# Kernel optimization log

Measured on AMD Instinct MI355X. Metric: run time of the kernel, lower is better.

Reference implementation:

```python
import jax, jax.numpy as jnp
import numpy as np

V, OOV, E, HE, HD, B, S, T = 50000, 100, 128, 256, 256, 32, 256, 16
NEG = -1e20


def lstm(x, W, U, b, h0, c0):
    # x: [B, L, F]; standard (Keras-style i,f,g,o) LSTM via scan over time
    def step(carry, xt):
        h, c = carry
        z = xt @ W + h @ U + b
        i, f, g, o = jnp.split(z, 4, axis=-1)
        c = jax.nn.sigmoid(f) * c + jax.nn.sigmoid(i) * jnp.tanh(g)
        h = jax.nn.sigmoid(o) * jnp.tanh(c)
        return (h, c), h
    (h, c), hs = jax.lax.scan(step, (h0, c0), jnp.swapaxes(x, 0, 1))
    return jnp.swapaxes(hs, 0, 1), h, c


def setup_inputs() -> dict:
    key = jax.random.key(0)
    ks = jax.random.split(key, 16)
    g = lambda i, shape: jax.random.normal(ks[i], shape, dtype=jnp.float32) * 0.05
    return {
        'x': jax.random.randint(ks[0], (B, S), 0, V),
        'x_with_oov': jax.random.randint(ks[1], (B, S), 0, V + OOV),
        'x_len': jax.random.randint(ks[2], (B,), 1, S + 1),
        'dec_x': jax.random.randint(ks[3], (B, T), 0, V),
        'embedding': g(4, (V, E)),
        'Wenc': g(5, (E, 4 * HE)), 'Uenc': g(6, (HE, 4 * HE)), 'benc': jnp.zeros(4 * HE, jnp.float32),
        'We2d': g(7, (HE, HD)), 'be2d': jnp.zeros(HD, jnp.float32),
        'Wdec': g(8, (E, 4 * HD)), 'Udec': g(9, (HD, 4 * HD)), 'bdec': jnp.zeros(4 * HD, jnp.float32),
        'Wattn': g(10, (HD, HE)),
        'Wout': g(11, (HE + HD, HD)), 'bout': jnp.zeros(HD, jnp.float32),
        'Wgen': g(12, (HD, V)),
        'Wcopy': g(13, (HE, HD)), 'bcopy': jnp.zeros(HD, jnp.float32),
    }


def reference(x, x_with_oov, x_len, dec_x, embedding, Wenc, Uenc, benc,
              We2d, be2d, Wdec, Udec, bdec, Wattn, Wout, bout, Wgen, Wcopy, bcopy):
    # Encoder (unidirectional; Keras encoder ignores mask in this branch)
    enc_out, eh, ec = lstm(embedding[x], Wenc, Uenc, benc,
                           jnp.zeros((B, HE), embedding.dtype), jnp.zeros((B, HE), embedding.dtype))
    # NOTE: source applies encoder2decoder_state to BOTH h and c (faithful)
    h0 = eh @ We2d + be2d
    c0 = ec @ We2d + be2d
    # Decoder LSTM
    dec_out, sh, sc = lstm(embedding[dec_x], Wdec, Udec, bdec, h0, c0)  # [B,T,HD]
    mask = jnp.arange(S)[None, :] < x_len[:, None]                      # [B,S]
    # Attention (score_mode='general')
    scores = jnp.einsum('bth,he,bse->bts', dec_out, Wattn, enc_out)     # [B,T,S]
    scores = jnp.where(mask[:, None, :], scores, NEG)
    aw = jax.nn.softmax(scores, axis=2)
    ctx = jnp.einsum('bts,bse->bte', aw, enc_out)                       # [B,T,HE]
    attn_out = jnp.tanh(jnp.concatenate([ctx, dec_out], axis=-1) @ Wout + bout)  # [B,T,HD]
    # Generation scores, padded with tiny constant over OOV slots
    gen = jnp.exp(attn_out @ Wgen)                                      # [B,T,V]
    gen = jnp.pad(gen, ((0, 0), (0, 0), (0, OOV)), constant_values=1e-10)
    # Copy scores over source positions, scattered into extended vocab
    copy_seq = jnp.einsum('bsh,bth->bts', jnp.tanh(enc_out @ Wcopy + bcopy), attn_out)
    copy_seq = jnp.exp(jnp.where(mask[:, None, :], copy_seq, NEG))      # [B,T,S]
    b_idx = jnp.arange(B)[:, None, None]
    t_idx = jnp.arange(T)[None, :, None]
    v_idx = x_with_oov[:, None, :]                                      # broadcast to [B,T,S]
    copy_vocab = jnp.zeros((B, T, V + OOV), gen.dtype).at[b_idx, t_idx, v_idx].add(copy_seq)
    total = gen + copy_vocab
    log_prob = jnp.log(total / jnp.sum(total, axis=2, keepdims=True))
    return log_prob, sh, sc
```

## Files before the change

### kernel.cpp

```cpp
#include <hip/hip_runtime.h>

#define V_   50000
#define OOV_ 100
#define VO_  50100
#define E_   128
#define HE_  256
#define HD_  256
#define B_   32
#define S_   256
#define T_   16

typedef _Float16 h2_t __attribute__((ext_vector_type(2)));
typedef __attribute__((ext_vector_type(8))) short bfrag_t;
typedef __attribute__((ext_vector_type(4))) float f32x4;
typedef unsigned short ushort_t;

union U32H2 { unsigned u; h2_t h; };
union FRAG  { uint4 u; bfrag_t s; };

static __device__ __forceinline__ float bf2f(unsigned short b) {
  return __uint_as_float(((unsigned)b) << 16);
}
static __device__ __forceinline__ unsigned short f2bf(float f) {
  unsigned u = __float_as_uint(f);
  unsigned r = (u + 0x7fffu + ((u >> 16) & 1u)) >> 16;
  return (unsigned short)r;
}
static __device__ __forceinline__ float sigm(float x) { return 1.f / (1.f + expf(-x)); }
static __device__ __forceinline__ float fast_sigm(float z) {
  float e = __builtin_amdgcn_exp2f(-1.442695041f * z);
  return __builtin_amdgcn_rcpf(1.f + e);
}
static __device__ __forceinline__ float fast_tanh(float z) {
  float e = __builtin_amdgcn_exp2f(-2.885390082f * z);
  return 2.f * __builtin_amdgcn_rcpf(1.f + e) - 1.f;
}

static __device__ __forceinline__ float dot2u(unsigned upair, unsigned hpairv, float acc) {
  U32H2 a; a.u = upair;
  U32H2 b; b.u = hpairv;
#if __has_builtin(__builtin_amdgcn_fdot2)
  return __builtin_amdgcn_fdot2(a.h, b.h, acc, false);
#else
  acc = fmaf((float)a.h.x, (float)b.h.x, acc);
  return fmaf((float)a.h.y, (float)b.h.y, acc);
#endif
}

__global__ __launch_bounds__(256) void mfma_gemm(
    const ushort_t* __restrict__ A, const ushort_t* __restrict__ Bt,
    const float* __restrict__ bias, float* __restrict__ C, ushort_t* __restrict__ Cbf,
    float* __restrict__ rsum, int M, int N, int K, int ldC, int act)
{
  const int w = threadIdx.x >> 6, lane = threadIdx.x & 63;
  const int m0 = blockIdx.y * 64 + w * 16;
  const int n0 = blockIdx.x * 64;
  const int l16 = lane & 15, lq = lane >> 4;
  f32x4 acc[4] = {f32x4{0,0,0,0}, f32x4{0,0,0,0}, f32x4{0,0,0,0}, f32x4{0,0,0,0}};
  for (int k0 = 0; k0 < K; k0 += 32) {
    FRAG a;
    a.u = *(const uint4*)(A + (size_t)(m0 + l16) * K + k0 + lq * 8);
#pragma unroll
    for (int ns = 0; ns < 4; ns++) {
      int n = n0 + ns * 16 + l16;
      int nc = n < N ? n : N - 1;
      FRAG bf;
      bf.u = *(const uint4*)(Bt + (size_t)nc * K + k0 + lq * 8);
      acc[ns] = __builtin_amdgcn_mfma_f32_16x16x32_bf16(a.s, bf.s, acc[ns], 0, 0, 0);
    }
  }
  float bv[4];
#pragma unroll
  for (int ns = 0; ns < 4; ns++) {
    int col = n0 + ns * 16 + l16;
    bv[ns] = (bias && col < N) ? bias[col] : 0.f;
  }
#pragma unroll
  for (int r = 0; r < 4; r++) {
    int row = m0 + lq * 4 + r;
    float part = 0.f;
#pragma unroll
    for (int ns = 0; ns < 4; ns++) {
      int col = n0 + ns * 16 + l16;
      if (col < N) {
        float v = acc[ns][r] + bv[ns];
        if (act == 1) v = tanhf(v);
        else if (act == 2) v = expf(v);
        if (Cbf) Cbf[(size_t)row * ldC + col] = f2bf(v);
        else     C[(size_t)row * ldC + col] = v;
        part += v;
      }
    }
    if (rsum) {
      part += __shfl_xor(part, 1);
      part += __shfl_xor(part, 2);
      part += __shfl_xor(part, 4);
      part += __shfl_xor(part, 8);
      if (l16 == 0) atomicAdd(&rsum[row], part);
    }
  }
}

static __device__ __forceinline__ void tconv_tile(
    const float* __restrict__ W, ushort_t* __restrict__ Wt, int K, int N,
    int kb, int nb, int tid, ushort_t (*tile)[33])
{
  const int tx = tid & 31, ty = tid >> 5;
#pragma unroll
  for (int p = 0; p < 4; p++) {
    int k = kb + ty + p * 8, n = nb + tx;
    if (k < K && n < N) tile[ty + p * 8][tx] = f2bf(W[(size_t)k * N + n]);
  }
  __syncthreads();
#pragma unroll
  for (int p = 0; p < 4; p++) {
    int n = nb + ty + p * 8, k = kb + tx;
    if (k < K && n < N) Wt[(size_t)n * K + k] = tile[tx][ty + p * 8];
  }
}
static __device__ __forceinline__ void packU2_one(
    const float* __restrict__ U, unsigned* __restrict__ out, int i)
{
  int p = i >> 10, col = i & 1023;
  U32H2 cv; cv.h = h2_t{(_Float16)U[(size_t)(2 * p) * 1024 + col],
                        (_Float16)U[(size_t)(2 * p + 1) * 1024 + col]};
  out[i] = cv.u;
}

__global__ __launch_bounds__(256) void prep_kernel(
    const float* __restrict__ Wenc, const float* __restrict__ Wdec,
    const float* __restrict__ We2d, const float* __restrict__ Wattn,
    const float* __restrict__ Wout, const float* __restrict__ Wcopy,
    const float* __restrict__ Uenc, const float* __restrict__ Udec,
    const int* __restrict__ x, const int* __restrict__ decx, const float* __restrict__ emb,
    ushort_t* WencT, ushort_t* WdecT, ushort_t* We2dT, ushort_t* WattnT,
    ushort_t* WoutT, ushort_t* WcopyT, unsigned* Upk2E, unsigned* Upk2D,
    ushort_t* xembbf, ushort_t* dembbf)
{
  __shared__ ushort_t tile[32][33];
  int blk = blockIdx.x;
  const int tid = threadIdx.x;
  if (blk < 128) { tconv_tile(Wenc, WencT, 128, 1024, (blk >> 5) * 32, (blk & 31) * 32, tid, tile); return; }
  blk -= 128;
  if (blk < 128) { tconv_tile(Wdec, WdecT, 128, 1024, (blk >> 5) * 32, (blk & 31) * 32, tid, tile); return; }
  blk -= 128;
  if (blk < 64)  { tconv_tile(We2d, We2dT, 256, 256, (blk >> 3) * 32, (blk & 7) * 32, tid, tile); return; }
  blk -= 64;
  if (blk < 64)  { tconv_tile(Wattn, WattnT, 256, 256, (blk >> 3) * 32, (blk & 7) * 32, tid, tile); return; }
  blk -= 64;
  if (blk < 128) { tconv_tile(Wout, WoutT, 512, 256, (blk >> 3) * 32, (blk & 7) * 32, tid, tile); return; }
  blk -= 128;
  if (blk < 64)  { tconv_tile(Wcopy, WcopyT, 256, 256, (blk >> 3) * 32, (blk & 7) * 32, tid, tile); return; }
  blk -= 64;
  if (blk < 512) { packU2_one(Uenc, Upk2E, blk * 256 + tid); return; }
  blk -= 512;
  if (blk < 512) { packU2_one(Udec, Upk2D, blk * 256 + tid); return; }
  blk -= 512;
  if (blk < 4096) {
    int i = blk * 256 + tid, r = i >> 7;
    xembbf[i] = f2bf(emb[(size_t)x[r] * E_ + (i & 127)]);
    return;
  }
  blk -= 4096;
  {
    int i = blk * 256 + tid, r = i >> 7;
    dembbf[i] = f2bf(emb[(size_t)decx[r] * E_ + (i & 127)]);
  }
}

#define DOT8(u0, u1, hpi)                \
  acc[0] = dot2u(u0.x, hpi, acc[0]);     \
  acc[1] = dot2u(u0.y, hpi, acc[1]);     \
  acc[2] = dot2u(u0.z, hpi, acc[2]);     \
  acc[3] = dot2u(u0.w, hpi, acc[3]);     \
  acc[4] = dot2u(u1.x, hpi, acc[4]);     \
  acc[5] = dot2u(u1.y, hpi, acc[5]);     \
  acc[6] = dot2u(u1.z, hpi, acc[6]);     \
  acc[7] = dot2u(u1.w, hpi, acc[7]);

__global__
__attribute__((amdgpu_flat_work_group_size(1024, 1024), amdgpu_waves_per_eu(4, 4)))
void lstm12(
    const float* __restrict__ Xpre, const unsigned* __restrict__ Upk2,
    const float* __restrict__ h0, const float* __restrict__ c0,
    ushort_t* __restrict__ outH, float* __restrict__ hN, float* __restrict__ cN,
    ushort_t* __restrict__ hNbf, ushort_t* __restrict__ cNbf,
    int steps, const float* __restrict__ Wg, ushort_t* __restrict__ WgT)
{
  __shared__ unsigned ldsU[8 * 4096];
  __shared__ float    zpart[4 * 1028];
  __shared__ unsigned hpair[8 * 20];
  const int tid = threadIdx.x;

  if (blockIdx.x >= 32) {
    ushort_t* tile = (ushort_t*)ldsU;
    int tb = blockIdx.x - 32;
    int kb = (tb & 3) * 64, nb = (tb >> 2) * 64;
#pragma unroll
    for (int p = 0; p < 4; p++) {
      int i = p * 1024 + tid, k = i >> 6, n = i & 63;
      if (nb + n < V_) tile[k * 65 + n] = f2bf(Wg[(size_t)(kb + k) * V_ + nb + n]);
    }
    __syncthreads();
#pragma unroll
    for (int p = 0; p < 4; p++) {
      int i = p * 1024 + tid, n = i >> 6, k = i & 63;
      if (nb + n < V_) WgT[(size_t)(nb + n) * 256 + kb + k] = tile[k * 65 + n];
    }
    return;
  }

  const int b = blockIdx.x;
  const int jg = tid >> 3, kq = tid & 7;

  uint4 Ur[24];
  const unsigned* ubase = Upk2 + jg * 8;
#pragma unroll
  for (int i = 0; i < 12; i++) {
    int p = kq * 16 + i;
    Ur[2 * i]     = *(const uint4*)(ubase + p * 1024);
    Ur[2 * i + 1] = *(const uint4*)(ubase + p * 1024 + 4);
  }
  {
    unsigned* myst = &ldsU[tid * 4];
#pragma unroll
    for (int i = 0; i < 4; i++) {
      int p = kq * 16 + 12 + i;
      uint4 q0 = *(const uint4*)(ubase + p * 1024);
      uint4 q1 = *(const uint4*)(ubase + p * 1024 + 4);
      *(uint4*)(myst + (2 * i) * 4096)     = q0;
      *(uint4*)(myst + (2 * i + 1) * 4096) = q1;
    }
  }
  float c = 0.f, hcur = 0.f;
  if (tid < 256) {
    c    = c0 ? c0[b * 256 + tid] : 0.f;
    hcur = h0 ? h0[b * 256 + tid] : 0.f;
  }
  if (tid < 128) {
    float a  = h0 ? h0[b * 256 + 2 * tid] : 0.f;
    float b2 = h0 ? h0[b * 256 + 2 * tid + 1] : 0.f;
    U32H2 cv; cv.h = h2_t{(_Float16)a, (_Float16)b2};
    hpair[(tid >> 4) * 20 + (tid & 15)] = cv.u;
  }
  __syncthreads();

  const float* xp = Xpre + (size_t)b * steps * 1024;
  const unsigned* myld = &ldsU[tid * 4];

  for (int t = 0; t < steps; t++) {
    float xq0 = 0.f, xq1 = 0.f, xq2 = 0.f, xq3 = 0.f;
    if (tid < 256) {
      const float* xr = xp + (size_t)t * 1024 + tid;
      xq0 = xr[0]; xq1 = xr[256]; xq2 = xr[512]; xq3 = xr[768];
    }
    float acc[8] = {0.f, 0.f, 0.f, 0.f, 0.f, 0.f, 0.f, 0.f};
    {
      uint4 hA = *(const uint4*)&hpair[kq * 20];
      DOT8(Ur[0], Ur[1], hA.x)  DOT8(Ur[2], Ur[3], hA.y)
      DOT8(Ur[4], Ur[5], hA.z)  DOT8(Ur[6], Ur[7], hA.w)
    }
    {
      uint4 hB = *(const uint4*)&hpair[kq * 20 + 4];
      DOT8(Ur[8], Ur[9], hB.x)   DOT8(Ur[10], Ur[11], hB.y)
      DOT8(Ur[12], Ur[13], hB.z) DOT8(Ur[14], Ur[15], hB.w)
    }
    {
      uint4 hC = *(const uint4*)&hpair[kq * 20 + 8];
      DOT8(Ur[16], Ur[17], hC.x) DOT8(Ur[18], Ur[19], hC.y)
      DOT8(Ur[20], Ur[21], hC.z) DOT8(Ur[22], Ur[23], hC.w)
    }
    {
      uint4 hD = *(const uint4*)&hpair[kq * 20 + 12];
      unsigned hh[4] = {hD.x, hD.y, hD.z, hD.w};
#pragma unroll
      for (int r = 0; r < 4; r++) {
        uint4 u0 = *(const uint4*)(myld + (2 * r) * 4096);
        uint4 u1 = *(const uint4*)(myld + (2 * r + 1) * 4096);
        unsigned hpi = hh[r];
        DOT8(u0, u1, hpi)
      }
    }
#pragma unroll
    for (int g = 0; g < 8; g++) acc[g] += __shfl_xor(acc[g], 1);
    if ((kq & 1) == 0) {
      int r = kq >> 1;
      *(float4*)&zpart[r * 1028 + jg * 8]     = make_float4(acc[0], acc[1], acc[2], acc[3]);
      *(float4*)&zpart[r * 1028 + jg * 8 + 4] = make_float4(acc[4], acc[5], acc[6], acc[7]);
    }
    __syncthreads();
    if (tid < 256) {
      float zi = xq0, zf = xq1, zg = xq2, zo = xq3;
#pragma unroll
      for (int r = 0; r < 4; r++) {
        const float* zr = &zpart[r * 1028 + tid];
        zi += zr[0]; zf += zr[256]; zg += zr[512]; zo += zr[768];
      }
      float ai = fast_sigm(zi), af = fast_sigm(zf);
      float ag = fast_tanh(zg), ao = fast_sigm(zo);
      c = fmaf(af, c, ai * ag);
      hcur = ao * fast_tanh(c);
      outH[((size_t)b * steps + t) * 256 + tid] = f2bf(hcur);
      float hnx = __shfl_down(hcur, 1);
      if ((tid & 1) == 0) {
        U32H2 cv; cv.h = h2_t{(_Float16)hcur, (_Float16)hnx};
        int P = tid >> 1;
        hpair[(P >> 4) * 20 + (P & 15)] = cv.u;
      }
    }
    __syncthreads();
  }
  if (tid < 256) {
    if (hN)   hN[b * 256 + tid] = hcur;
    if (cN)   cN[b * 256 + tid] = c;
    if (hNbf) hNbf[b * 256 + tid] = f2bf(hcur);
    if (cNbf) cNbf[b * 256 + tid] = f2bf(c);
  }
}

__global__ __launch_bounds__(256) void attn_kernel(
    const float* __restrict__ dq, const ushort_t* __restrict__ enc,
    const int* __restrict__ x_len, const ushort_t* __restrict__ dec,
    ushort_t* __restrict__ catb)
{
  __shared__ float q[256];
  __shared__ float eb[32][256];
  __shared__ float sc[256];
  __shared__ float red[8];
  const int bt = blockIdx.x, tid = threadIdx.x;
  const int b = bt >> 4;
  q[tid] = dq[(size_t)bt * 256 + tid];
  const int len = x_len[b];
  const unsigned* encu = (const unsigned*)(enc + (size_t)b * S_ * 256);
  __syncthreads();
  const int s_loc = tid >> 3, hb = (tid & 7) * 32;
  for (int cch = 0; cch < 8; cch++) {
#pragma unroll
    for (int qv = 0; qv < 16; qv++) {
      int idx = qv * 256 + tid;
      unsigned u = encu[cch * 4096 + idx];
      int row = idx >> 7, cp2 = (idx & 127) * 2;
      eb[row][cp2]     = bf2f((unsigned short)(u & 0xffffu));
      eb[row][cp2 + 1] = bf2f((unsigned short)(u >> 16));
    }
    __syncthreads();
    float p = 0.f;
#pragma unroll
    for (int h = 0; h < 32; h++) p = fmaf(q[hb + h], eb[s_loc][hb + h], p);
    p += __shfl_down(p, 4, 8);
    p += __shfl_down(p, 2, 8);
    p += __shfl_down(p, 1, 8);
    if ((tid & 7) == 0) sc[cch * 32 + s_loc] = p;
    __syncthreads();
  }
  float my = (tid < len) ? sc[tid] : -1e30f;
  float m = my;
#pragma unroll
  for (int o = 32; o >= 1; o >>= 1) m = fmaxf(m, __shfl_xor(m, o));
  if ((tid & 63) == 0) red[tid >> 6] = m;
  __syncthreads();
  float bm = fmaxf(fmaxf(red[0], red[1]), fmaxf(red[2], red[3]));
  float e = expf(my - bm);
  float s = e;
#pragma unroll
  for (int o = 32; o >= 1; o >>= 1) s += __shfl_xor(s, o);
  if ((tid & 63) == 0) red[4 + (tid >> 6)] = s;
  __syncthreads();
  float tot = red[4] + red[5] + red[6] + red[7];
  sc[tid] = e / tot;
  __syncthreads();
  const ushort_t* encb = enc + (size_t)b * S_ * 256;
  float acc = 0.f;
  for (int s2 = 0; s2 < 256; s2++) acc = fmaf(sc[s2], bf2f(encb[(size_t)s2 * 256 + tid]), acc);
  catb[(size_t)bt * 512 + tid]       = f2bf(acc);
  catb[(size_t)bt * 512 + 256 + tid] = dec[(size_t)bt * 256 + tid];
}

__global__ __launch_bounds__(256) void copyseq_kernel(
    const ushort_t* __restrict__ at, const ushort_t* __restrict__ cp,
    const int* __restrict__ x_len, float* __restrict__ cseq)
{
  __shared__ float q[256];
  __shared__ float eb[32][256];
  __shared__ float sc[256];
  const int bt = blockIdx.x, tid = threadIdx.x;
  const int b = bt >> 4;
  q[tid] = bf2f(at[(size_t)bt * 256 + tid]);
  const int len = x_len[b];
  const unsigned* cpu_ = (const unsigned*)(cp + (size_t)b * S_ * 256);
  __syncthreads();
  const int s_loc = tid >> 3, hb = (tid & 7) * 32;
  for (int cch = 0; cch < 8; cch++) {
#pragma unroll
    for (int qv = 0; qv < 16; qv++) {
      int idx = qv * 256 + tid;
      unsigned u = cpu_[cch * 4096 + idx];
      int row = idx >> 7, cp2 = (idx & 127) * 2;
      eb[row][cp2]     = bf2f((unsigned short)(u & 0xffffu));
      eb[row][cp2 + 1] = bf2f((unsigned short)(u >> 16));
    }
    __syncthreads();
    float p = 0.f;
#pragma unroll
    for (int h = 0; h < 32; h++) p = fmaf(q[hb + h], eb[s_loc][hb + h], p);
    p += __shfl_down(p, 4, 8);
    p += __shfl_down(p, 2, 8);
    p += __shfl_down(p, 1, 8);
    if ((tid & 7) == 0) sc[cch * 32 + s_loc] = p;
    __syncthreads();
  }
  cseq[(size_t)bt * 256 + tid] = (tid < len) ? expf(sc[tid]) : 0.f;
}

__global__ __launch_bounds__(256) void scatter_kernel(
    const float* __restrict__ cseq, const int* __restrict__ xoov,
    float* __restrict__ out, float* __restrict__ rsum)
{
  __shared__ float red[4];
  const int bt = blockIdx.x, tid = threadIdx.x, b = bt >> 4;
  if (tid < OOV_) out[(size_t)bt * VO_ + V_ + tid] = 1e-10f;
  __syncthreads();
  float v = cseq[(size_t)bt * 256 + tid];
  if (v != 0.f) atomicAdd(&out[(size_t)bt * VO_ + xoov[b * S_ + tid]], v);
  float s = v;
#pragma unroll
  for (int o = 32; o >= 1; o >>= 1) s += __shfl_xor(s, o);
  if ((tid & 63) == 0) red[tid >> 6] = s;
  __syncthreads();
  if (tid == 0) atomicAdd(&rsum[bt], red[0] + red[1] + red[2] + red[3]);
}
__global__ void rowlog_kernel(const float* __restrict__ rsum, float* __restrict__ rowlog) {
  int i = blockIdx.x * 256 + threadIdx.x;
  if (i < B_ * T_) rowlog[i] = logf(rsum[i] + 1e-8f);
}
__global__ void finalize_kernel(float* __restrict__ out, const float* __restrict__ rowlog) {
  size_t i = (size_t)blockIdx.x * 256 + threadIdx.x;
  if (i < (size_t)B_ * T_ * VO_) {
    int bt = (int)(i / VO_);
    out[i] = logf(out[i]) - rowlog[bt];
  }
}

extern "C" void kernel_launch(void* const* d_in, const int* in_sizes, int n_in,
                              void* d_out, int out_size, void* d_ws, size_t ws_size,
                              hipStream_t stream) {
  const int*   x     = (const int*)d_in[0];
  const int*   xoov  = (const int*)d_in[1];
  const int*   xlen  = (const int*)d_in[2];
  const int*   decx  = (const int*)d_in[3];
  const float* emb   = (const float*)d_in[4];
  const float* Wenc  = (const float*)d_in[5];
  const float* Uenc  = (const float*)d_in[6];
  const float* benc  = (const float*)d_in[7];
  const float* We2d  = (const float*)d_in[8];
  const float* be2d  = (const float*)d_in[9];
  const float* Wdec  = (const float*)d_in[10];
  const float* Udec  = (const float*)d_in[11];
  const float* bdec  = (const float*)d_in[12];
  const float* Wattn = (const float*)d_in[13];
  const float* Wout  = (const float*)d_in[14];
  const float* bout  = (const float*)d_in[15];
  const float* Wgen  = (const float*)d_in[16];
  const float* Wcopy = (const float*)d_in[17];
  const float* bcopy = (const float*)d_in[18];
  float* out = (float*)d_out;
  float* ws  = (float*)d_ws;

  float*    Xenc   = ws + 0;
  ushort_t* WgenT  = (ushort_t*)(ws + 0);
  ushort_t* cp_bf  = (ushort_t*)(ws + 6400000);
  float*    dqb    = ws + 8388608;
  float*    cseq   = ws + 8781824;
  float*    rsum   = ws + 8912896;
  float*    rowlog = ws + 8913408;
  ushort_t* Abf    = (ushort_t*)(ws + 8913920);
  ushort_t* catb   = (ushort_t*)(ws + 8979456);
  ushort_t* decObf = (ushort_t*)(ws + 9110528);
  ushort_t* xembbf = (ushort_t*)(ws + 9176064);
  ushort_t* dembbf = (ushort_t*)(ws + 9700352);
  float*    Xdec   = ws + 9733120;
  ushort_t* WencT  = (ushort_t*)(ws + 10257408);
  ushort_t* WdecT  = (ushort_t*)(ws + 10322944);
  ushort_t* We2dT  = (ushort_t*)(ws + 10388480);
  ushort_t* WattnT = (ushort_t*)(ws + 10421248);
  ushort_t* WoutT  = (ushort_t*)(ws + 10454016);
  ushort_t* WcopyT = (ushort_t*)(ws + 10519552);
  unsigned* Upk2E  = (unsigned*)(ws + 10552320);
  unsigned* Upk2D  = (unsigned*)(ws + 10683392);
  ushort_t* encObf = (ushort_t*)(ws + 10814464);
  float*    ehc    = ws + 11863040;
  ushort_t* ehcbf  = (ushort_t*)(ws + 11879424);
  float*    h0c0   = ws + 11887616;

  float* sh  = out + (size_t)B_ * T_ * VO_;
  float* scf = sh + B_ * HD_;

  hipMemsetAsync(rsum, 0, 512 * sizeof(float), stream);

  hipLaunchKernelGGL(prep_kernel, dim3(5952), dim3(256), 0, stream,
                     Wenc, Wdec, We2d, Wattn, Wout, Wcopy, Uenc, Udec, x, decx, emb,
                     WencT, WdecT, We2dT, WattnT, WoutT, WcopyT, Upk2E, Upk2D,
                     xembbf, dembbf);

  hipLaunchKernelGGL(mfma_gemm, dim3(16, 128), dim3(256), 0, stream,
                     xembbf, WencT, benc, Xenc, (ushort_t*)nullptr, (float*)nullptr,
                     B_ * S_, 1024, 128, 1024, 0);
  hipLaunchKernelGGL(mfma_gemm, dim3(16, 8), dim3(256), 0, stream,
                     dembbf, WdecT, bdec, Xdec, (ushort_t*)nullptr, (float*)nullptr,
                     B_ * T_, 1024, 128, 1024, 0);

  hipLaunchKernelGGL(lstm12, dim3(32), dim3(1024), 0, stream,
                     Xenc, Upk2E, (const float*)nullptr, (const float*)nullptr,
                     encObf, (float*)nullptr, (float*)nullptr,
                     ehcbf, ehcbf + 32 * 256, S_,
                     (const float*)nullptr, (ushort_t*)nullptr);

  hipLaunchKernelGGL(mfma_gemm, dim3(4, 1), dim3(256), 0, stream,
                     ehcbf, We2dT, be2d, h0c0, (ushort_t*)nullptr, (float*)nullptr,
                     64, 256, 256, 256, 0);

  hipLaunchKernelGGL(lstm12, dim3(32 + 3128), dim3(1024), 0, stream,
                     Xdec, Upk2D, h0c0, h0c0 + 32 * 256, decObf, sh, scf,
                     (ushort_t*)nullptr, (ushort_t*)nullptr, T_,
                     Wgen, WgenT);

  hipLaunchKernelGGL(mfma_gemm, dim3(4, 8), dim3(256), 0, stream,
                     decObf, WattnT, (const float*)nullptr, dqb, (ushort_t*)nullptr,
                     (float*)nullptr, B_ * T_, 256, 256, 256, 0);
  hipLaunchKernelGGL(attn_kernel, dim3(B_ * T_), dim3(256), 0, stream,
                     dqb, encObf, xlen, decObf, catb);
  hipLaunchKernelGGL(mfma_gemm, dim3(4, 8), dim3(256), 0, stream,
                     catb, WoutT, bout, (float*)nullptr, Abf, (float*)nullptr,
                     B_ * T_, 256, 512, 256, 1);
  hipLaunchKernelGGL(mfma_gemm, dim3(4, 128), dim3(256), 0, stream,
                     encObf, WcopyT, bcopy, (float*)nullptr, cp_bf, (float*)nullptr,
                     B_ * S_, 256, 256, 256, 1);
  hipLaunchKernelGGL(mfma_gemm, dim3(782, 8), dim3(256), 0, stream,
                     Abf, WgenT, (const float*)nullptr, out, (ushort_t*)nullptr, rsum,
                     B_ * T_, V_, 256, VO_, 2);
  hipLaunchKernelGGL(copyseq_kernel, dim3(B_ * T_), dim3(256), 0, stream, Abf, cp_bf, xlen, cseq);
  hipLaunchKernelGGL(scatter_kernel, dim3(512), dim3(256), 0, stream, cseq, xoov, out, rsum);
  hipLaunchKernelGGL(rowlog_kernel, dim3(2), dim3(256), 0, stream, rsum, rowlog);
  hipLaunchKernelGGL(finalize_kernel, dim3((B_ * T_ * VO_ + 255) / 256), dim3(256), 0, stream,
                     out, rowlog);
}
```

Before: 1.188 ms.

## Fuse Wgen bf16 conversion into a dedicated vocab GEMM, drop transpose pass

```diff
diff --git a/kernel.cpp b/kernel.cpp
--- a/kernel.cpp
+++ b/kernel.cpp
@@ -92,6 +92,64 @@
       }
     }
     if (rsum) {
+      part += __shfl_xor(part, 1);
+      part += __shfl_xor(part, 2);
+      part += __shfl_xor(part, 4);
+      part += __shfl_xor(part, 8);
+      if (l16 == 0) atomicAdd(&rsum[row], part);
+    }
+  }
+}
+
+__global__ __launch_bounds__(256) void wgen_gemm(
+    const ushort_t* __restrict__ A, const float* __restrict__ Wg,
+    float* __restrict__ out, float* __restrict__ rsum)
+{
+  __shared__ ushort_t ldsB[64 * 264];
+  const int tid = threadIdx.x;
+  const int n0 = blockIdx.x * 64;
+#pragma unroll
+  for (int it = 0; it < 16; it++) {
+    int idx = it * 256 + tid;
+    int k = idx >> 4, c4 = idx & 15;
+    int nsrc = n0 + c4 * 4;
+    if (nsrc > V_ - 4) nsrc = V_ - 4;
+    float4 f = *(const float4*)&Wg[(size_t)k * V_ + nsrc];
+    ldsB[(c4 * 4 + 0) * 264 + k] = f2bf(f.x);
+    ldsB[(c4 * 4 + 1) * 264 + k] = f2bf(f.y);
+    ldsB[(c4 * 4 + 2) * 264 + k] = f2bf(f.z);
+    ldsB[(c4 * 4 + 3) * 264 + k] = f2bf(f.w);
+  }
+  __syncthreads();
+  const int w = tid >> 6, lane = tid & 63;
+  const int l16 = lane & 15, lq = lane >> 4;
+  for (int mt = 0; mt < 8; mt++) {
+    const int mb = mt * 64 + w * 16;
+    f32x4 acc[4] = {f32x4{0,0,0,0}, f32x4{0,0,0,0}, f32x4{0,0,0,0}, f32x4{0,0,0,0}};
+#pragma unroll
+    for (int k0 = 0; k0 < 256; k0 += 32) {
+      FRAG a;
+      a.u = *(const uint4*)(A + (size_t)(mb + l16) * 256 + k0 + lq * 8);
+#pragma unroll
+      for (int ns = 0; ns < 4; ns++) {
+        FRAG bf;
+        bf.u = *(const uint4*)&ldsB[(ns * 16 + l16) * 264 + k0 + lq * 8];
+        acc[ns] = __builtin_amdgcn_mfma_f32_16x16x32_bf16(a.s, bf.s, acc[ns], 0, 0, 0);
+      }
+    }
+#pragma unroll
+    for (int r = 0; r < 4; r++) {
+      int row = mb + lq * 4 + r;
+      float part = 0.f;
+#pragma unroll
+      for (int ns = 0; ns < 4; ns++) {
+        int col = n0 + ns * 16 + l16;
+        if (col < V_) {
+          float v = expf(acc[ns][r]);
+          out[(size_t)row * VO_ + col] = v;
+          part += v;
+        }
+      }
       part += __shfl_xor(part, 1);
       part += __shfl_xor(part, 2);
       part += __shfl_xor(part, 4);
@@ -185,30 +243,12 @@
     const float* __restrict__ h0, const float* __restrict__ c0,
     ushort_t* __restrict__ outH, float* __restrict__ hN, float* __restrict__ cN,
     ushort_t* __restrict__ hNbf, ushort_t* __restrict__ cNbf,
-    int steps, const float* __restrict__ Wg, ushort_t* __restrict__ WgT)
+    int steps)
 {
   __shared__ unsigned ldsU[8 * 4096];
   __shared__ float    zpart[4 * 1028];
   __shared__ unsigned hpair[8 * 20];
   const int tid = threadIdx.x;
-
-  if (blockIdx.x >= 32) {
-    ushort_t* tile = (ushort_t*)ldsU;
-    int tb = blockIdx.x - 32;
-    int kb = (tb & 3) * 64, nb = (tb >> 2) * 64;
-#pragma unroll
-    for (int p = 0; p < 4; p++) {
-      int i = p * 1024 + tid, k = i >> 6, n = i & 63;
-      if (nb + n < V_) tile[k * 65 + n] = f2bf(Wg[(size_t)(kb + k) * V_ + nb + n]);
-    }
-    __syncthreads();
-#pragma unroll
-    for (int p = 0; p < 4; p++) {
-      int i = p * 1024 + tid, n = i >> 6, k = i & 63;
-      if (nb + n < V_) WgT[(size_t)(nb + n) * 256 + kb + k] = tile[k * 65 + n];
-    }
-    return;
-  }
 
   const int b = blockIdx.x;
   const int jg = tid >> 3, kq = tid & 7;
@@ -467,7 +507,6 @@
   float* ws  = (float*)d_ws;
 
   float*    Xenc   = ws + 0;
-  ushort_t* WgenT  = (ushort_t*)(ws + 0);
   ushort_t* cp_bf  = (ushort_t*)(ws + 6400000);
   float*    dqb    = ws + 8388608;
   float*    cseq   = ws + 8781824;
@@ -488,7 +527,6 @@
   unsigned* Upk2E  = (unsigned*)(ws + 10552320);
   unsigned* Upk2D  = (unsigned*)(ws + 10683392);
   ushort_t* encObf = (ushort_t*)(ws + 10814464);
-  float*    ehc    = ws + 11863040;
   ushort_t* ehcbf  = (ushort_t*)(ws + 11879424);
   float*    h0c0   = ws + 11887616;
 
@@ -512,17 +550,15 @@
   hipLaunchKernelGGL(lstm12, dim3(32), dim3(1024), 0, stream,
                      Xenc, Upk2E, (const float*)nullptr, (const float*)nullptr,
                      encObf, (float*)nullptr, (float*)nullptr,
-                     ehcbf, ehcbf + 32 * 256, S_,
-                     (const float*)nullptr, (ushort_t*)nullptr);
+                     ehcbf, ehcbf + 32 * 256, S_);
 
   hipLaunchKernelGGL(mfma_gemm, dim3(4, 1), dim3(256), 0, stream,
                      ehcbf, We2dT, be2d, h0c0, (ushort_t*)nullptr, (float*)nullptr,
                      64, 256, 256, 256, 0);
 
-  hipLaunchKernelGGL(lstm12, dim3(32 + 3128), dim3(1024), 0, stream,
+  hipLaunchKernelGGL(lstm12, dim3(32), dim3(1024), 0, stream,
                      Xdec, Upk2D, h0c0, h0c0 + 32 * 256, decObf, sh, scf,
-                     (ushort_t*)nullptr, (ushort_t*)nullptr, T_,
-                     Wgen, WgenT);
+                     (ushort_t*)nullptr, (ushort_t*)nullptr, T_);
 
   hipLaunchKernelGGL(mfma_gemm, dim3(4, 8), dim3(256), 0, stream,
                      decObf, WattnT, (const float*)nullptr, dqb, (ushort_t*)nullptr,
@@ -535,9 +571,8 @@
   hipLaunchKernelGGL(mfma_gemm, dim3(4, 128), dim3(256), 0, stream,
                      encObf, WcopyT, bcopy, (float*)nullptr, cp_bf, (float*)nullptr,
                      B_ * S_, 256, 256, 256, 1);
-  hipLaunchKernelGGL(mfma_gemm, dim3(782, 8), dim3(256), 0, stream,
-                     Abf, WgenT, (const float*)nullptr, out, (ushort_t*)nullptr, rsum,
-                     B_ * T_, V_, 256, VO_, 2);
+  hipLaunchKernelGGL(wgen_gemm, dim3(782), dim3(256), 0, stream,
+                     Abf, Wgen, out, rsum);
   hipLaunchKernelGGL(copyseq_kernel, dim3(B_ * T_), dim3(256), 0, stream, Abf, cp_bf, xlen, cseq);
   hipLaunchKernelGGL(scatter_kernel, dim3(512), dim3(256), 0, stream, cseq, xoov, out, rsum);
   hipLaunchKernelGGL(rowlog_kernel, dim3(2), dim3(256), 0, stream, rsum, rowlog);
```

After: 1.105 ms. 7.0% less time.
